# Performance work log

Hardware: AMD Instinct MI355X
Metric: run time of the kernel (lower is better)

## Reference

```python
import jax, jax.numpy as jnp
import numpy as np

N, D, L, B = 100000, 1024, 128, 16
EPS = 1e-16  # torch_geometric softmax denominator eps


def setup_inputs() -> dict:
    key = jax.random.key(0)
    k_feat, k_b, k_wa, k_wb, k_wc = jax.random.split(key, 5)
    feature = jax.random.normal(k_feat, (N, D), dtype=jnp.float32)
    batch = jnp.sort(jax.random.randint(k_b, (N,), 0, B, dtype=jnp.int64))
    # xavier_normal_ init for the three Linear layers
    std_a = float(np.sqrt(2.0 / (D + L)))
    std_c = float(np.sqrt(2.0 / (L + 1)))
    Wa = jax.random.normal(k_wa, (L, D), dtype=jnp.float32) * std_a
    Wb = jax.random.normal(k_wb, (L, D), dtype=jnp.float32) * std_a
    Wc = jax.random.normal(k_wc, (1, L), dtype=jnp.float32) * std_c
    ba = jnp.zeros((L,), jnp.float32)
    bb = jnp.zeros((L,), jnp.float32)
    bc = jnp.zeros((1,), jnp.float32)
    return {"feature": feature, "batch": batch, "Wa": Wa, "ba": ba,
            "Wb": Wb, "bb": bb, "Wc": Wc, "bc": bc}


def reference(feature, batch, Wa, ba, Wb, bb, Wc, bc):
    # gated score MLP
    a = jax.nn.sigmoid(feature @ Wa.T + ba)          # [N, L]
    b = jnp.tanh(feature @ Wb.T + bb)                # [N, L]
    score = (a * b) @ Wc.T + bc                      # [N, 1]
    # segment softmax over bags (torch_geometric.utils.softmax)
    s = score[:, 0]                                  # [N]
    seg_max = jax.ops.segment_max(s, batch, num_segments=B)   # [B]
    e = jnp.exp(s - seg_max[batch])                  # [N]
    denom = jax.ops.segment_sum(e, batch, num_segments=B)     # [B]
    score_softmax = (e / (denom[batch] + EPS))[:, None]       # [N, 1]
    # scatter-sum weighted features per bag
    out = jax.ops.segment_sum(score_softmax * feature, batch, num_segments=B)  # [B, D]
    return (out, score, score_softmax, feature)
```

## Files before the change

kernel.cpp:

```cpp
#include <hip/hip_runtime.h>
#include <hip/hip_bf16.h>
#include <cmath>

#define NROWS 100000
#define DIM   1024
#define LH    128
#define NSEG  16
#define EPSF  1e-16f

#define OUT_OFF   0
#define SCORE_OFF (NSEG * DIM)
#define SM_OFF    (SCORE_OFF + NROWS)
#define FEAT_OFF  (SM_OFF + NROWS)

typedef __attribute__((ext_vector_type(4))) float floatx4;
typedef __attribute__((ext_vector_type(8))) short shortx8;

__device__ __forceinline__ unsigned short f2bf(float x) {
    unsigned u = __float_as_uint(x);
    u += 0x7FFFu + ((u >> 16) & 1u);
    return (unsigned short)(u >> 16);
}
__device__ __forceinline__ unsigned enc_f32(float f) {
    unsigned u = __float_as_uint(f);
    return (u & 0x80000000u) ? ~u : (u | 0x80000000u);
}
__device__ __forceinline__ float dec_f32(unsigned e) {
    unsigned u = (e & 0x80000000u) ? (e ^ 0x80000000u) : ~e;
    return __uint_as_float(u);
}

__global__ void init_kernel(const float* __restrict__ Wa,
                            const float* __restrict__ Wb,
                            unsigned short* __restrict__ wbf,
                            unsigned* __restrict__ segmax,
                            float* __restrict__ denom,
                            float* __restrict__ out) {
    int idx = blockIdx.x * 256 + threadIdx.x;
    if (idx < LH * DIM)
        wbf[idx] = f2bf(Wa[idx]);
    else if (idx < 2 * LH * DIM)
        wbf[idx] = f2bf(Wb[idx - LH * DIM]);
    if (idx < NSEG * DIM) out[OUT_OFF + idx] = 0.f;
    if (idx < NSEG) { segmax[idx] = 0u; denom[idx] = 0.f; }
}

__launch_bounds__(256)
__global__ void score_kernel(const float* __restrict__ feature,
                             const int* __restrict__ batch,
                             const unsigned short* __restrict__ wbf,
                             const float* __restrict__ ba,
                             const float* __restrict__ bb,
                             const float* __restrict__ wc,
                             const float* __restrict__ bc,
                             float* __restrict__ outp,
                             unsigned* __restrict__ segmax) {
    __shared__ __align__(16) unsigned short sA[64][72];
    __shared__ __align__(16) unsigned short sW[256][72];
    __shared__ float sBias[3 * LH];
    __shared__ float sScore[64];
    __shared__ int   sBatch[64];
    __shared__ unsigned sMax[NSEG];

    const int tid  = threadIdx.x;
    const int wave = tid >> 6;
    const int lane = tid & 63;
    const int q    = lane >> 4;
    const int c    = lane & 15;
    const int row0 = blockIdx.x * 64;

    if (tid < LH) {
        sBias[tid]          = ba[tid];
        sBias[LH + tid]     = bb[tid];
        sBias[2 * LH + tid] = wc[tid];
    }
    if (tid < NSEG) sMax[tid] = 0u;

    floatx4 acc[16];
#pragma unroll
    for (int t = 0; t < 16; ++t)
#pragma unroll
        for (int i = 0; i < 4; ++i) acc[t][i] = 0.f;

    for (int k0 = 0; k0 < DIM; k0 += 64) {
        __syncthreads();
        {
            const int rr = tid >> 4;
            const int cc = (tid & 15) << 2;
#pragma unroll
            for (int p = 0; p < 4; ++p) {
                const int r    = p * 16 + rr;
                const int grow = row0 + r;
                floatx4 v; v[0] = v[1] = v[2] = v[3] = 0.f;
                if (grow < NROWS) {
                    v = *(const floatx4*)(feature + (size_t)grow * DIM + k0 + cc);
                    *(floatx4*)(outp + FEAT_OFF + (size_t)grow * DIM + k0 + cc) = v;
                }
                sA[r][cc + 0] = f2bf(v[0]);
                sA[r][cc + 1] = f2bf(v[1]);
                sA[r][cc + 2] = f2bf(v[2]);
                sA[r][cc + 3] = f2bf(v[3]);
            }
        }
        {
#pragma unroll
            for (int p = 0; p < 8; ++p) {
                const int chunk = p * 256 + tid;
                const int r  = chunk >> 3;
                const int cc = (chunk & 7) << 3;
                shortx8 v = *(const shortx8*)(wbf + (size_t)r * DIM + k0 + cc);
                *(shortx8*)&sW[r][cc] = v;
            }
        }
        __syncthreads();
#pragma unroll
        for (int ks = 0; ks < 2; ++ks) {
            const int kk = ks * 32 + q * 8;
            shortx8 a = *(const shortx8*)&sA[wave * 16 + c][kk];
#pragma unroll
            for (int t = 0; t < 16; ++t) {
                shortx8 b = *(const shortx8*)&sW[t * 16 + c][kk];
                acc[t] = __builtin_amdgcn_mfma_f32_16x16x32_bf16(a, b, acc[t], 0, 0, 0);
            }
        }
    }

    float p4[4] = {0.f, 0.f, 0.f, 0.f};
#pragma unroll
    for (int t = 0; t < 8; ++t) {
        const int col = t * 16 + c;
        const float bav = sBias[col];
        const float bbv = sBias[LH + col];
        const float wcv = sBias[2 * LH + col];
#pragma unroll
        for (int i = 0; i < 4; ++i) {
            float u = acc[t][i] + bav;
            float v = acc[t + 8][i] + bbv;
            float sg = 1.f / (1.f + __expf(-u));
            float th = tanhf(v);
            p4[i] += sg * th * wcv;
        }
    }
#pragma unroll
    for (int i = 0; i < 4; ++i) {
        p4[i] += __shfl_xor(p4[i], 1, 16);
        p4[i] += __shfl_xor(p4[i], 2, 16);
        p4[i] += __shfl_xor(p4[i], 4, 16);
        p4[i] += __shfl_xor(p4[i], 8, 16);
    }

    __syncthreads();
    if (tid < 64) sBatch[tid] = -1;
    __syncthreads();

    const float bcv = bc[0];
    if (c == 0) {
#pragma unroll
        for (int i = 0; i < 4; ++i) {
            const int r    = wave * 16 + q * 4 + i;
            const int grow = row0 + r;
            if (grow < NROWS) {
                const float s = p4[i] + bcv;
                outp[SCORE_OFF + grow] = s;
                sScore[r] = s;
                sBatch[r] = batch[grow];
            }
        }
    }
    __syncthreads();
    if (tid < 64 && sBatch[tid] >= 0)
        atomicMax(&sMax[sBatch[tid]], enc_f32(sScore[tid]));
    __syncthreads();
    if (tid < NSEG && sMax[tid] != 0u)
        atomicMax(&segmax[tid], sMax[tid]);
}

__global__ void exp_kernel(const float* __restrict__ score,
                           const int* __restrict__ batch,
                           const unsigned* __restrict__ segmax,
                           float* __restrict__ evals,
                           float* __restrict__ denom) {
    __shared__ float sden[NSEG];
    const int tid = threadIdx.x;
    const int idx = blockIdx.x * 256 + tid;
    if (tid < NSEG) sden[tid] = 0.f;
    __syncthreads();
    if (idx < NROWS) {
        const int b = batch[idx];
        const float m = dec_f32(segmax[b]);
        const float e = expf(score[idx] - m);
        evals[idx] = e;
        atomicAdd(&sden[b], e);
    }
    __syncthreads();
    if (tid < NSEG && sden[tid] != 0.f) atomicAdd(&denom[tid], sden[tid]);
}

__launch_bounds__(256)
__global__ void wsum_kernel(const float* __restrict__ feature,
                            const int* __restrict__ batch,
                            const float* __restrict__ denom,
                            float* __restrict__ evals,
                            float* __restrict__ outp) {
    __shared__ float sw[128];
    __shared__ int   sb[128];
    const int tid = threadIdx.x;
    const int r0  = blockIdx.x * 128;

    if (tid < 128) {
        const int row = r0 + tid;
        if (row < NROWS) {
            const int b = batch[row];
            const float w = evals[row] / (denom[b] + EPSF);
            evals[row] = w;
            sw[tid] = w;
            sb[tid] = b;
        } else {
            sw[tid] = 0.f;
            sb[tid] = -1;
        }
    }
    __syncthreads();

    floatx4 acc; acc[0] = acc[1] = acc[2] = acc[3] = 0.f;
    int curseg = -1;
    const int cc = tid * 4;
    for (int r = 0; r < 128; ++r) {
        const int b = sb[r];
        if (b < 0) break;
        if (b != curseg) {
            if (curseg >= 0) {
#pragma unroll
                for (int j = 0; j < 4; ++j)
                    atomicAdd(&outp[OUT_OFF + curseg * DIM + cc + j], acc[j]);
            }
            curseg = b;
            acc[0] = acc[1] = acc[2] = acc[3] = 0.f;
        }
        const floatx4 f = *(const floatx4*)(feature + (size_t)(r0 + r) * DIM + cc);
        const float w = sw[r];
        acc[0] += w * f[0];
        acc[1] += w * f[1];
        acc[2] += w * f[2];
        acc[3] += w * f[3];
    }
    if (curseg >= 0) {
#pragma unroll
        for (int j = 0; j < 4; ++j)
            atomicAdd(&outp[OUT_OFF + curseg * DIM + cc + j], acc[j]);
    }
}

extern "C" void kernel_launch(void* const* d_in, const int* in_sizes, int n_in,
                              void* d_out, int out_size, void* d_ws, size_t ws_size,
                              hipStream_t stream) {
    const float* feature = (const float*)d_in[0];
    const int*   batch   = (const int*)d_in[1];
    const float* Wa      = (const float*)d_in[2];
    const float* ba      = (const float*)d_in[3];
    const float* Wb      = (const float*)d_in[4];
    const float* bb      = (const float*)d_in[5];
    const float* Wc      = (const float*)d_in[6];
    const float* bc      = (const float*)d_in[7];
    float* out = (float*)d_out;

    unsigned short* wbf = (unsigned short*)d_ws;
    unsigned* segmax = (unsigned*)((char*)d_ws + 2 * LH * DIM * 2);
    float*    denom  = (float*)((char*)d_ws + 2 * LH * DIM * 2 + 64);

    init_kernel<<<(2 * LH * DIM) / 256, 256, 0, stream>>>(Wa, Wb, wbf, segmax, denom, out);
    score_kernel<<<(NROWS + 63) / 64, 256, 0, stream>>>(feature, batch, wbf, ba, bb, Wc, bc, out, segmax);
    exp_kernel<<<(NROWS + 255) / 256, 256, 0, stream>>>(out + SCORE_OFF, batch, segmax, out + SM_OFF, denom);
    wsum_kernel<<<(NROWS + 127) / 128, 256, 0, stream>>>(feature, batch, denom, out + SM_OFF, out);
}
```

Before: 1.031 ms.

## Pre-swizzle weights into MFMA layout, load A fragments to registers, fast-path wsum

The init kernel now converts Wa/Wb to bf16 in the exact per-lane MFMA fragment order, grouped by 64-wide k chunk. The score kernel copies each chunk straight into LDS with global_load_lds. It drops the A tile in LDS: each lane loads its own feature row slice into registers, converts it to bf16, and writes the feature copy from there. The aim is to cut LDS traffic, bank conflicts and VALU conversion work in the GEMM main loop. The weighted-sum kernel adds a branch-free unrolled path for blocks whose rows all belong to one segment. The cost is less coalesced per-lane global reads of feature rows, plus reliance on correct waits for the async LDS loads.

After: 932.5 us. 9.5% less time.

```diff
diff --git a/kernel.cpp b/kernel.cpp
--- a/kernel.cpp
+++ b/kernel.cpp
@@ -1,5 +1,4 @@
 #include <hip/hip_runtime.h>
-#include <hip/hip_bf16.h>
 #include <cmath>
 
 #define NROWS 100000
@@ -28,6 +27,11 @@
 __device__ __forceinline__ float dec_f32(unsigned e) {
     unsigned u = (e & 0x80000000u) ? (e ^ 0x80000000u) : ~e;
     return __uint_as_float(u);
+}
+__device__ __forceinline__ void gload_lds16(const void* g, void* l) {
+    __builtin_amdgcn_global_load_lds(
+        (const __attribute__((address_space(1))) void*)g,
+        (__attribute__((address_space(3))) void*)l, 16, 0, 0);
 }
 
 __global__ void init_kernel(const float* __restrict__ Wa,
@@ -36,11 +40,28 @@
                             unsigned* __restrict__ segmax,
                             float* __restrict__ denom,
                             float* __restrict__ out) {
-    int idx = blockIdx.x * 256 + threadIdx.x;
-    if (idx < LH * DIM)
-        wbf[idx] = f2bf(Wa[idx]);
-    else if (idx < 2 * LH * DIM)
-        wbf[idx] = f2bf(Wb[idx - LH * DIM]);
+    const int idx = blockIdx.x * 256 + threadIdx.x;
+    {
+        const int r  = idx >> 7;
+        const int kg = idx & 127;
+        const int k  = kg << 3;
+        const float* src = (r < LH) ? (Wa + (size_t)r * DIM + k)
+                                    : (Wb + (size_t)(r - LH) * DIM + k);
+        const floatx4 v0 = *(const floatx4*)src;
+        const floatx4 v1 = *(const floatx4*)(src + 4);
+        const int chunk = kg >> 3;
+        const int ks    = (kg >> 2) & 1;
+        const int q     = kg & 3;
+        const int t     = r >> 4;
+        const int c     = r & 15;
+        shortx8 o;
+        o[0] = (short)f2bf(v0[0]); o[1] = (short)f2bf(v0[1]);
+        o[2] = (short)f2bf(v0[2]); o[3] = (short)f2bf(v0[3]);
+        o[4] = (short)f2bf(v1[0]); o[5] = (short)f2bf(v1[1]);
+        o[6] = (short)f2bf(v1[2]); o[7] = (short)f2bf(v1[3]);
+        *(shortx8*)(wbf + (size_t)chunk * 16384 + t * 1024 + ks * 512
+                        + (q * 16 + c) * 8) = o;
+    }
     if (idx < NSEG * DIM) out[OUT_OFF + idx] = 0.f;
     if (idx < NSEG) { segmax[idx] = 0u; denom[idx] = 0.f; }
 }
@@ -55,19 +76,20 @@
                              const float* __restrict__ bc,
                              float* __restrict__ outp,
                              unsigned* __restrict__ segmax) {
-    __shared__ __align__(16) unsigned short sA[64][72];
-    __shared__ __align__(16) unsigned short sW[256][72];
+    __shared__ __align__(16) unsigned short sW[16384];
     __shared__ float sBias[3 * LH];
     __shared__ float sScore[64];
     __shared__ int   sBatch[64];
     __shared__ unsigned sMax[NSEG];
 
-    const int tid  = threadIdx.x;
-    const int wave = tid >> 6;
-    const int lane = tid & 63;
-    const int q    = lane >> 4;
-    const int c    = lane & 15;
-    const int row0 = blockIdx.x * 64;
+    const int tid   = threadIdx.x;
+    const int wave  = tid >> 6;
+    const int lane  = tid & 63;
+    const int q     = lane >> 4;
+    const int c     = lane & 15;
+    const int row0  = blockIdx.x * 64;
+    const int myrow = row0 + wave * 16 + c;
+    const bool inb  = myrow < NROWS;
 
     if (tid < LH) {
         sBias[tid]          = ba[tid];
@@ -82,45 +104,46 @@
 #pragma unroll
         for (int i = 0; i < 4; ++i) acc[t][i] = 0.f;
 
+    const float* arow = feature + (size_t)myrow * DIM;
+    float*       erow = outp + FEAT_OFF + (size_t)myrow * DIM;
+
     for (int k0 = 0; k0 < DIM; k0 += 64) {
         __syncthreads();
-        {
-            const int rr = tid >> 4;
-            const int cc = (tid & 15) << 2;
-#pragma unroll
-            for (int p = 0; p < 4; ++p) {
-                const int r    = p * 16 + rr;
-                const int grow = row0 + r;
-                floatx4 v; v[0] = v[1] = v[2] = v[3] = 0.f;
-                if (grow < NROWS) {
-                    v = *(const floatx4*)(feature + (size_t)grow * DIM + k0 + cc);
-                    *(floatx4*)(outp + FEAT_OFF + (size_t)grow * DIM + k0 + cc) = v;
-                }
-                sA[r][cc + 0] = f2bf(v[0]);
-                sA[r][cc + 1] = f2bf(v[1]);
-                sA[r][cc + 2] = f2bf(v[2]);
-                sA[r][cc + 3] = f2bf(v[3]);
+        const unsigned short* gsrc = wbf + (size_t)(k0 >> 6) * 16384;
+#pragma unroll
+        for (int p = 0; p < 8; ++p) {
+            const int off = (p * 256 + tid) * 8;
+            gload_lds16(gsrc + off, &sW[off]);
+        }
+        shortx8 afrag[2];
+#pragma unroll
+        for (int ks = 0; ks < 2; ++ks) {
+            const int kk = k0 + ks * 32 + q * 8;
+            floatx4 v0 = {0.f, 0.f, 0.f, 0.f};
+            floatx4 v1 = {0.f, 0.f, 0.f, 0.f};
+            if (inb) {
+                v0 = *(const floatx4*)(arow + kk);
+                v1 = *(const floatx4*)(arow + kk + 4);
+                *(floatx4*)(erow + kk)     = v0;
+                *(floatx4*)(erow + kk + 4) = v1;
             }
-        }
-        {
-#pragma unroll
-            for (int p = 0; p < 8; ++p) {
-                const int chunk = p * 256 + tid;
-                const int r  = chunk >> 3;
-                const int cc = (chunk & 7) << 3;
-                shortx8 v = *(const shortx8*)(wbf + (size_t)r * DIM + k0 + cc);
-                *(shortx8*)&sW[r][cc] = v;
-            }
+            afrag[ks][0] = (short)f2bf(v0[0]);
+            afrag[ks][1] = (short)f2bf(v0[1]);
+            afrag[ks][2] = (short)f2bf(v0[2]);
+            afrag[ks][3] = (short)f2bf(v0[3]);
+            afrag[ks][4] = (short)f2bf(v1[0]);
+            afrag[ks][5] = (short)f2bf(v1[1]);
+            afrag[ks][6] = (short)f2bf(v1[2]);
+            afrag[ks][7] = (short)f2bf(v1[3]);
         }
         __syncthreads();
 #pragma unroll
         for (int ks = 0; ks < 2; ++ks) {
-            const int kk = ks * 32 + q * 8;
-            shortx8 a = *(const shortx8*)&sA[wave * 16 + c][kk];
 #pragma unroll
             for (int t = 0; t < 16; ++t) {
-                shortx8 b = *(const shortx8*)&sW[t * 16 + c][kk];
-                acc[t] = __builtin_amdgcn_mfma_f32_16x16x32_bf16(a, b, acc[t], 0, 0, 0);
+                shortx8 b = *(const shortx8*)&sW[t * 1024 + ks * 512 + lane * 8];
+                acc[t] = __builtin_amdgcn_mfma_f32_16x16x32_bf16(afrag[ks], b,
+                                                                 acc[t], 0, 0, 0);
             }
         }
     }
@@ -222,32 +245,51 @@
     }
     __syncthreads();
 
+    const int cc = tid * 4;
+    const int b0 = sb[0];
+    const int bL = sb[127];
     floatx4 acc; acc[0] = acc[1] = acc[2] = acc[3] = 0.f;
-    int curseg = -1;
-    const int cc = tid * 4;
-    for (int r = 0; r < 128; ++r) {
-        const int b = sb[r];
-        if (b < 0) break;
-        if (b != curseg) {
-            if (curseg >= 0) {
-#pragma unroll
-                for (int j = 0; j < 4; ++j)
-                    atomicAdd(&outp[OUT_OFF + curseg * DIM + cc + j], acc[j]);
+
+    if (b0 == bL) {
+        const float* fp = feature + (size_t)r0 * DIM + cc;
+#pragma unroll 8
+        for (int r = 0; r < 128; ++r) {
+            const floatx4 f = *(const floatx4*)(fp + (size_t)r * DIM);
+            const float w = sw[r];
+            acc[0] += w * f[0];
+            acc[1] += w * f[1];
+            acc[2] += w * f[2];
+            acc[3] += w * f[3];
+        }
+#pragma unroll
+        for (int j = 0; j < 4; ++j)
+            atomicAdd(&outp[OUT_OFF + b0 * DIM + cc + j], acc[j]);
+    } else {
+        int curseg = -1;
+        for (int r = 0; r < 128; ++r) {
+            const int b = sb[r];
+            if (b < 0) break;
+            if (b != curseg) {
+                if (curseg >= 0) {
+#pragma unroll
+                    for (int j = 0; j < 4; ++j)
+                        atomicAdd(&outp[OUT_OFF + curseg * DIM + cc + j], acc[j]);
+                }
+                curseg = b;
+                acc[0] = acc[1] = acc[2] = acc[3] = 0.f;
             }
-            curseg = b;
-            acc[0] = acc[1] = acc[2] = acc[3] = 0.f;
-        }
-        const floatx4 f = *(const floatx4*)(feature + (size_t)(r0 + r) * DIM + cc);
-        const float w = sw[r];
-        acc[0] += w * f[0];
-        acc[1] += w * f[1];
-        acc[2] += w * f[2];
-        acc[3] += w * f[3];
-    }
-    if (curseg >= 0) {
-#pragma unroll
-        for (int j = 0; j < 4; ++j)
-            atomicAdd(&outp[OUT_OFF + curseg * DIM + cc + j], acc[j]);
+            const floatx4 f = *(const floatx4*)(feature + (size_t)(r0 + r) * DIM + cc);
+            const float w = sw[r];
+            acc[0] += w * f[0];
+            acc[1] += w * f[1];
+            acc[2] += w * f[2];
+            acc[3] += w * f[3];
+        }
+        if (curseg >= 0) {
+#pragma unroll
+            for (int j = 0; j < 4; ++j)
+                atomicAdd(&outp[OUT_OFF + curseg * DIM + cc + j], acc[j]);
+        }
     }
 }
 
@@ -268,7 +310,7 @@
     unsigned* segmax = (unsigned*)((char*)d_ws + 2 * LH * DIM * 2);
     float*    denom  = (float*)((char*)d_ws + 2 * LH * DIM * 2 + 64);
 
-    init_kernel<<<(2 * LH * DIM) / 256, 256, 0, stream>>>(Wa, Wb, wbf, segmax, denom, out);
+    init_kernel<<<128, 256, 0, stream>>>(Wa, Wb, wbf, segmax, denom, out);
     score_kernel<<<(NROWS + 63) / 64, 256, 0, stream>>>(feature, batch, wbf, ba, bb, Wc, bc, out, segmax);
     exp_kernel<<<(NROWS + 255) / 256, 256, 0, stream>>>(out + SCORE_OFF, batch, segmax, out + SM_OFF, denom);
     wsum_kernel<<<(NROWS + 127) / 128, 256, 0, stream>>>(feature, batch, denom, out + SM_OFF, out);
```
